# Kernel optimization log

Measured on AMD Instinct MI355X. Metric: run time of the kernel, lower is better.

The kernel has to match this reference:

```python
import jax, jax.numpy as jnp
import numpy as np
import math

B, N, D = 2, 4096, 1024
NUM_LAYERS = 12
INIT_RANGE = 0.02


def setup_inputs() -> dict:
    key = jax.random.key(0)
    k1, k2 = jax.random.split(key)
    hidden_states = jax.random.normal(k1, (B, N, D), dtype=jnp.float32)
    std = INIT_RANGE / math.sqrt(2.0 * NUM_LAYERS * D)
    queries = jax.random.normal(k2, (D, D), dtype=jnp.float32) * std
    return {"hidden_states": hidden_states, "queries": queries}


def reference(hidden_states, queries):
    # Q = F.linear(X, W) = X @ W^T  -> [B, N, D]
    q = jnp.einsum('bnd,ed->bne', hidden_states, queries)
    # pre_attn = Q @ X^T  -> [B, N, N]
    pre_attn = jnp.einsum('bne,bme->bnm', q, hidden_states)
    # attention = pre_attn @ X  -> [B, N, D]
    attention = jnp.einsum('bnm,bmd->bnd', pre_attn, hidden_states)
    return attention
```

## Files before the change

### kernel.cpp

```cpp
#include <hip/hip_runtime.h>
#include <hip/hip_bf16.h>
#include <stdint.h>

using bf16 = __hip_bfloat16;
typedef __attribute__((ext_vector_type(8))) short short8;
typedef __attribute__((ext_vector_type(4))) float f32x4;

#define BM 128
#define BN 128
#define BK 32

__device__ __forceinline__ void g2lds16(const void* g, void* l) {
    __builtin_amdgcn_global_load_lds(
        (const __attribute__((address_space(1))) void*)g,
        (__attribute__((address_space(3))) void*)l,
        16, 0, 0);
}

__device__ __forceinline__ short f2bs(float x) {
    union { bf16 h; short s; } u;
    u.h = __float2bfloat16(x);
    return u.s;
}

__device__ __forceinline__ int bswz(int row, int cg) { return cg ^ ((row >> 1) & 3); }
__device__ __forceinline__ int fswz(int row, int cg) { return cg ^ (row & 7); }

__global__ __launch_bounds__(256)
void transpose_cvt(const float* __restrict__ src, ushort* __restrict__ dst,
                   int R, int C, long sstride, long dstride)
{
    __shared__ __align__(16) ushort t[64][72];
    const float* s = src + (size_t)blockIdx.z * sstride;
    ushort*      d = dst + (size_t)blockIdx.z * dstride;
    const int r0 = blockIdx.y * 64, c0 = blockIdx.x * 64;
    const int tid = threadIdx.x;
#pragma unroll
    for (int ii = 0; ii < 4; ++ii) {
        int idx = ii * 256 + tid;
        int r = idx >> 4, c4 = (idx & 15) * 4;
        float4 v = *(const float4*)&s[(size_t)(r0 + r) * C + c0 + c4];
        union { ushort u[4]; uint2 q; } o;
        o.u[0] = (ushort)f2bs(v.x); o.u[1] = (ushort)f2bs(v.y);
        o.u[2] = (ushort)f2bs(v.z); o.u[3] = (ushort)f2bs(v.w);
        *(uint2*)&t[r][c4] = o.q;
    }
    __syncthreads();
#pragma unroll
    for (int ii = 0; ii < 2; ++ii) {
        int idx = ii * 256 + tid;
        int c = idx >> 3, r8 = (idx & 7) * 8;
        union { ushort u[8]; uint4 v; } tmp;
#pragma unroll
        for (int j = 0; j < 8; ++j) tmp.u[j] = t[r8 + j][c];
        *(uint4*)&d[(size_t)(c0 + c) * R + r0 + r8] = tmp.v;
    }
}

__global__ __launch_bounds__(256)
void cvt_f32_bf16(const float* __restrict__ in, ushort* __restrict__ out, int n4)
{
    int i = blockIdx.x * 256 + threadIdx.x;
    if (i >= n4) return;
    float4 v = ((const float4*)in)[i];
    union { ushort u[4]; uint2 q; } o;
    o.u[0] = (ushort)f2bs(v.x); o.u[1] = (ushort)f2bs(v.y);
    o.u[2] = (ushort)f2bs(v.z); o.u[3] = (ushort)f2bs(v.w);
    ((uint2*)out)[i] = o.q;
}

template <int MODE, int A_F32>
__global__ __launch_bounds__(256)
void gemm_bt(const void* __restrict__ Av, const bf16* __restrict__ B,
             void* __restrict__ Cv, int M, int N, int K, int kChunks,
             long sA, long sB, long sC)
{
    __shared__ __align__(16) bf16 lA[BM * BK * (A_F32 ? 2 : 1)];
    __shared__ __align__(16) bf16 lB[BN * BK];

    const int z     = blockIdx.z;
    const int batch = z / kChunks;
    const int chunk = z - batch * kChunks;
    const int kLen  = K / kChunks;
    const int k0    = chunk * kLen;

    const int m0 = blockIdx.y * BM;
    const int n0 = blockIdx.x * BN;

    const int tid  = threadIdx.x;
    const int lane = tid & 63;
    const int wave = tid >> 6;
    const int wr   = wave >> 1, wc = wave & 1;
    const int ml   = lane & 15;
    const int q    = lane >> 4;

    const bf16* Bb = B + (size_t)batch * sB;
    const bf16* bp[2];
#pragma unroll
    for (int s = 0; s < 2; ++s) {
        int idx = s * 256 + tid;
        int row = idx >> 2, cg = idx & 3;
        bp[s] = Bb + (size_t)(n0 + row) * K + k0 + 8 * bswz(row, cg);
    }

    const float* a32[4];
    const bf16*  a16[2];
    if constexpr (A_F32) {
        const float* Ab = (const float*)Av + (size_t)batch * sA;
#pragma unroll
        for (int s = 0; s < 4; ++s) {
            int idx = s * 256 + tid;
            int row = idx >> 3, cg = idx & 7;
            a32[s] = Ab + (size_t)(m0 + row) * K + k0 + 4 * fswz(row, cg);
        }
    } else {
        const bf16* Ab = (const bf16*)Av + (size_t)batch * sA;
#pragma unroll
        for (int s = 0; s < 2; ++s) {
            int idx = s * 256 + tid;
            int row = idx >> 2, cg = idx & 3;
            a16[s] = Ab + (size_t)(m0 + row) * K + k0 + 8 * bswz(row, cg);
        }
    }

    f32x4 acc[4][4] = {};

    const int nk = kLen / BK;
    for (int kt = 0; kt < nk; ++kt) {
        if constexpr (A_F32) {
            float* lAf = (float*)lA;
#pragma unroll
            for (int s = 0; s < 4; ++s) {
                g2lds16(a32[s], &lAf[(s * 256 + tid) * 4]);
                a32[s] += BK;
            }
        } else {
#pragma unroll
            for (int s = 0; s < 2; ++s) {
                g2lds16(a16[s], &lA[(s * 256 + tid) * 8]);
                a16[s] += BK;
            }
        }
#pragma unroll
        for (int s = 0; s < 2; ++s) {
            g2lds16(bp[s], &lB[(s * 256 + tid) * 8]);
            bp[s] += BK;
        }
        __syncthreads();

        short8 af[4], bfr[4];
#pragma unroll
        for (int i = 0; i < 4; ++i) {
            const int rA = wr * 64 + i * 16 + ml;
            const int rB = wc * 64 + i * 16 + ml;
            if constexpr (A_F32) {
                const float* lAf = (const float*)lA;
                float4 x0 = *(const float4*)&lAf[rA * 32 + 4 * fswz(rA, 2 * q)];
                float4 x1 = *(const float4*)&lAf[rA * 32 + 4 * fswz(rA, 2 * q + 1)];
                af[i][0] = f2bs(x0.x); af[i][1] = f2bs(x0.y);
                af[i][2] = f2bs(x0.z); af[i][3] = f2bs(x0.w);
                af[i][4] = f2bs(x1.x); af[i][5] = f2bs(x1.y);
                af[i][6] = f2bs(x1.z); af[i][7] = f2bs(x1.w);
            } else {
                af[i] = *(const short8*)&lA[rA * 32 + 8 * bswz(rA, q)];
            }
            bfr[i] = *(const short8*)&lB[rB * 32 + 8 * bswz(rB, q)];
        }
#pragma unroll
        for (int mi = 0; mi < 4; ++mi)
#pragma unroll
            for (int ni = 0; ni < 4; ++ni)
                acc[mi][ni] = __builtin_amdgcn_mfma_f32_16x16x32_bf16(
                    af[mi], bfr[ni], acc[mi][ni], 0, 0, 0);
        __syncthreads();
    }

#pragma unroll
    for (int mi = 0; mi < 4; ++mi)
#pragma unroll
        for (int ni = 0; ni < 4; ++ni)
#pragma unroll
            for (int r = 0; r < 4; ++r) {
                int row = m0 + wr * 64 + mi * 16 + q * 4 + r;
                int col = n0 + wc * 64 + ni * 16 + ml;
                if constexpr (MODE == 1) {
                    float* Cf = (float*)Cv + (size_t)batch * sC;
                    atomicAdd(&Cf[(size_t)row * N + col], acc[mi][ni][r]);
                } else if constexpr (MODE == 0) {
                    ushort* Cb = (ushort*)Cv + (size_t)batch * sC;
                    Cb[(size_t)row * N + col] = (ushort)f2bs(acc[mi][ni][r]);
                } else {
                    float* Cf = (float*)Cv + (size_t)batch * sC;
                    Cf[(size_t)row * N + col] = acc[mi][ni][r];
                }
            }
}

extern "C" void kernel_launch(void* const* d_in, const int* in_sizes, int n_in,
                              void* d_out, int out_size, void* d_ws, size_t ws_size,
                              hipStream_t stream)
{
    const int B = 2, N = 4096, D = 1024;
    const float* X = (const float*)d_in[0];
    const float* W = (const float*)d_in[1];
    float* out = (float*)d_out;

    char* ob = (char*)d_out;
    ushort* Xt = (ushort*)ob;
    float*  Gf = (float*)(ob + (16ll << 20));
    ushort* G  = (ushort*)(ob + (24ll << 20));
    ushort* Wt = (ushort*)(ob + (28ll << 20));
    ushort* Mt = (ushort*)d_ws;

    transpose_cvt<<<dim3(D / 64, N / 64, B), 256, 0, stream>>>(
        X, Xt, N, D, (long)N * D, (long)D * N);
    transpose_cvt<<<dim3(D / 64, D / 64, 1), 256, 0, stream>>>(
        W, Wt, D, D, 0, 0);
    (void)hipMemsetAsync(Gf, 0, (size_t)B * D * D * sizeof(float), stream);
    gemm_bt<1, 0><<<dim3(D / BN, D / BM, B * 4), 256, 0, stream>>>(
        (const void*)Xt, (const bf16*)Xt, Gf, D, D, N, 4,
        (long)D * N, (long)D * N, (long)D * D);
    cvt_f32_bf16<<<dim3((B * D * D / 4 + 255) / 256), 256, 0, stream>>>(
        Gf, G, B * D * D / 4);
    gemm_bt<0, 0><<<dim3(D / BN, D / BM, B), 256, 0, stream>>>(
        (const void*)G, (const bf16*)Wt, Mt, D, D, D, 1,
        (long)D * D, 0, (long)D * D);
    gemm_bt<2, 1><<<dim3(D / BN, N / BM, B), 256, 0, stream>>>(
        (const void*)X, (const bf16*)Mt, out, N, D, D, 1,
        (long)N * D, (long)D * D, (long)N * D);
}
```

Baseline: 205.6 us.

## Halve GEMM N-tile and pre-convert X to bf16 in transpose pass

Makes the GEMM N-tile width a template parameter and uses 128x64 tiles for all three GEMMs, doubling the block count to improve occupancy and CU coverage on the small problems. The transpose kernel can also write a row-major bf16 copy of X into workspace when it is large enough. The final GEMM then reads bf16 A directly instead of loading fp32 and converting in its inner loop. The trade-offs are more B-tile reloads per unit of work, extra writes in the transpose kernel, and a dependence on workspace size.

```diff
diff --git a/kernel.cpp b/kernel.cpp
--- a/kernel.cpp
+++ b/kernel.cpp
@@ -7,7 +7,6 @@
 typedef __attribute__((ext_vector_type(4))) float f32x4;
 
 #define BM 128
-#define BN 128
 #define BK 32
 
 __device__ __forceinline__ void g2lds16(const void* g, void* l) {
@@ -27,12 +26,13 @@
 __device__ __forceinline__ int fswz(int row, int cg) { return cg ^ (row & 7); }
 
 __global__ __launch_bounds__(256)
-void transpose_cvt(const float* __restrict__ src, ushort* __restrict__ dst,
-                   int R, int C, long sstride, long dstride)
+void transpose_cvt(const float* __restrict__ src, ushort* __restrict__ dstT,
+                   ushort* __restrict__ dstN,
+                   int R, int C, long sstride, long dstrideT, long dstrideN)
 {
     __shared__ __align__(16) ushort t[64][72];
     const float* s = src + (size_t)blockIdx.z * sstride;
-    ushort*      d = dst + (size_t)blockIdx.z * dstride;
+    ushort*      dT = dstT + (size_t)blockIdx.z * dstrideT;
     const int r0 = blockIdx.y * 64, c0 = blockIdx.x * 64;
     const int tid = threadIdx.x;
 #pragma unroll
@@ -44,6 +44,10 @@
         o.u[0] = (ushort)f2bs(v.x); o.u[1] = (ushort)f2bs(v.y);
         o.u[2] = (ushort)f2bs(v.z); o.u[3] = (ushort)f2bs(v.w);
         *(uint2*)&t[r][c4] = o.q;
+        if (dstN) {
+            ushort* dN = dstN + (size_t)blockIdx.z * dstrideN;
+            *(uint2*)&dN[(size_t)(r0 + r) * C + c0 + c4] = o.q;
+        }
     }
     __syncthreads();
 #pragma unroll
@@ -53,7 +57,7 @@
         union { ushort u[8]; uint4 v; } tmp;
 #pragma unroll
         for (int j = 0; j < 8; ++j) tmp.u[j] = t[r8 + j][c];
-        *(uint4*)&d[(size_t)(c0 + c) * R + r0 + r8] = tmp.v;
+        *(uint4*)&dT[(size_t)(c0 + c) * R + r0 + r8] = tmp.v;
     }
 }
 
@@ -69,12 +73,14 @@
     ((uint2*)out)[i] = o.q;
 }
 
-template <int MODE, int A_F32>
+template <int MODE, int A_F32, int NFRAG>
 __global__ __launch_bounds__(256)
 void gemm_bt(const void* __restrict__ Av, const bf16* __restrict__ B,
              void* __restrict__ Cv, int M, int N, int K, int kChunks,
              long sA, long sB, long sC)
 {
+    constexpr int BN  = 32 * NFRAG;
+    constexpr int BSH = BN / 64;
     __shared__ __align__(16) bf16 lA[BM * BK * (A_F32 ? 2 : 1)];
     __shared__ __align__(16) bf16 lB[BN * BK];
 
@@ -95,9 +101,9 @@
     const int q    = lane >> 4;
 
     const bf16* Bb = B + (size_t)batch * sB;
-    const bf16* bp[2];
-#pragma unroll
-    for (int s = 0; s < 2; ++s) {
+    const bf16* bp[BSH];
+#pragma unroll
+    for (int s = 0; s < BSH; ++s) {
         int idx = s * 256 + tid;
         int row = idx >> 2, cg = idx & 3;
         bp[s] = Bb + (size_t)(n0 + row) * K + k0 + 8 * bswz(row, cg);
@@ -123,7 +129,7 @@
         }
     }
 
-    f32x4 acc[4][4] = {};
+    f32x4 acc[4][NFRAG] = {};
 
     const int nk = kLen / BK;
     for (int kt = 0; kt < nk; ++kt) {
@@ -142,17 +148,16 @@
             }
         }
 #pragma unroll
-        for (int s = 0; s < 2; ++s) {
+        for (int s = 0; s < BSH; ++s) {
             g2lds16(bp[s], &lB[(s * 256 + tid) * 8]);
             bp[s] += BK;
         }
         __syncthreads();
 
-        short8 af[4], bfr[4];
+        short8 af[4], bfr[NFRAG];
 #pragma unroll
         for (int i = 0; i < 4; ++i) {
             const int rA = wr * 64 + i * 16 + ml;
-            const int rB = wc * 64 + i * 16 + ml;
             if constexpr (A_F32) {
                 const float* lAf = (const float*)lA;
                 float4 x0 = *(const float4*)&lAf[rA * 32 + 4 * fswz(rA, 2 * q)];
@@ -164,34 +169,38 @@
             } else {
                 af[i] = *(const short8*)&lA[rA * 32 + 8 * bswz(rA, q)];
             }
-            bfr[i] = *(const short8*)&lB[rB * 32 + 8 * bswz(rB, q)];
+        }
+#pragma unroll
+        for (int j = 0; j < NFRAG; ++j) {
+            const int rB = wc * (16 * NFRAG) + j * 16 + ml;
+            bfr[j] = *(const short8*)&lB[rB * 32 + 8 * bswz(rB, q)];
         }
 #pragma unroll
         for (int mi = 0; mi < 4; ++mi)
 #pragma unroll
-            for (int ni = 0; ni < 4; ++ni)
-                acc[mi][ni] = __builtin_amdgcn_mfma_f32_16x16x32_bf16(
-                    af[mi], bfr[ni], acc[mi][ni], 0, 0, 0);
+            for (int nj = 0; nj < NFRAG; ++nj)
+                acc[mi][nj] = __builtin_amdgcn_mfma_f32_16x16x32_bf16(
+                    af[mi], bfr[nj], acc[mi][nj], 0, 0, 0);
         __syncthreads();
     }
 
 #pragma unroll
     for (int mi = 0; mi < 4; ++mi)
 #pragma unroll
-        for (int ni = 0; ni < 4; ++ni)
+        for (int nj = 0; nj < NFRAG; ++nj)
 #pragma unroll
             for (int r = 0; r < 4; ++r) {
                 int row = m0 + wr * 64 + mi * 16 + q * 4 + r;
-                int col = n0 + wc * 64 + ni * 16 + ml;
+                int col = n0 + wc * (16 * NFRAG) + nj * 16 + ml;
                 if constexpr (MODE == 1) {
                     float* Cf = (float*)Cv + (size_t)batch * sC;
-                    atomicAdd(&Cf[(size_t)row * N + col], acc[mi][ni][r]);
+                    atomicAdd(&Cf[(size_t)row * N + col], acc[mi][nj][r]);
                 } else if constexpr (MODE == 0) {
                     ushort* Cb = (ushort*)Cv + (size_t)batch * sC;
-                    Cb[(size_t)row * N + col] = (ushort)f2bs(acc[mi][ni][r]);
+                    Cb[(size_t)row * N + col] = (ushort)f2bs(acc[mi][nj][r]);
                 } else {
                     float* Cf = (float*)Cv + (size_t)batch * sC;
-                    Cf[(size_t)row * N + col] = acc[mi][ni][r];
+                    Cf[(size_t)row * N + col] = acc[mi][nj][r];
                 }
             }
 }
@@ -206,26 +215,36 @@
     float* out = (float*)d_out;
 
     char* ob = (char*)d_out;
+    char* ws = (char*)d_ws;
     ushort* Xt = (ushort*)ob;
     float*  Gf = (float*)(ob + (16ll << 20));
     ushort* G  = (ushort*)(ob + (24ll << 20));
     ushort* Wt = (ushort*)(ob + (28ll << 20));
-    ushort* Mt = (ushort*)d_ws;
+
+    const bool bigws = ws_size >= (20ull << 20);
+    ushort* Xb = bigws ? (ushort*)ws : nullptr;
+    ushort* Mt = (ushort*)(ws + (bigws ? (16ll << 20) : 0));
 
     transpose_cvt<<<dim3(D / 64, N / 64, B), 256, 0, stream>>>(
-        X, Xt, N, D, (long)N * D, (long)D * N);
+        X, Xt, Xb, N, D, (long)N * D, (long)D * N, (long)N * D);
     transpose_cvt<<<dim3(D / 64, D / 64, 1), 256, 0, stream>>>(
-        W, Wt, D, D, 0, 0);
+        W, Wt, nullptr, D, D, 0, 0, 0);
     (void)hipMemsetAsync(Gf, 0, (size_t)B * D * D * sizeof(float), stream);
-    gemm_bt<1, 0><<<dim3(D / BN, D / BM, B * 4), 256, 0, stream>>>(
+    gemm_bt<1, 0, 2><<<dim3(D / 64, D / BM, B * 4), 256, 0, stream>>>(
         (const void*)Xt, (const bf16*)Xt, Gf, D, D, N, 4,
         (long)D * N, (long)D * N, (long)D * D);
     cvt_f32_bf16<<<dim3((B * D * D / 4 + 255) / 256), 256, 0, stream>>>(
         Gf, G, B * D * D / 4);
-    gemm_bt<0, 0><<<dim3(D / BN, D / BM, B), 256, 0, stream>>>(
+    gemm_bt<0, 0, 2><<<dim3(D / 64, D / BM, B), 256, 0, stream>>>(
         (const void*)G, (const bf16*)Wt, Mt, D, D, D, 1,
         (long)D * D, 0, (long)D * D);
-    gemm_bt<2, 1><<<dim3(D / BN, N / BM, B), 256, 0, stream>>>(
-        (const void*)X, (const bf16*)Mt, out, N, D, D, 1,
-        (long)N * D, (long)D * D, (long)N * D);
-}
+    if (bigws) {
+        gemm_bt<2, 0, 2><<<dim3(D / 64, N / BM, B), 256, 0, stream>>>(
+            (const void*)Xb, (const bf16*)Mt, out, N, D, D, 1,
+            (long)N * D, (long)D * D, (long)N * D);
+    } else {
+        gemm_bt<2, 1, 2><<<dim3(D / 64, N / BM, B), 256, 0, stream>>>(
+            (const void*)X, (const bf16*)Mt, out, N, D, D, 1,
+            (long)N * D, (long)D * D, (long)N * D);
+    }
+}
```

Measured after the change: 196.6 us. 1.05x faster.
